# Performance work log

Measured on AMD Instinct MI355X. Metric: run time of the kernel, lower is better.

## Reference

```python
import jax, jax.numpy as jnp
import numpy as np

SEQ_LEN = 15
BATCH = 32
N_NODES = 5000
N_EDGES = 80000
IN_FEAT = 16
NHID = 2
G_FEAT = 1
HIDDEN = 512
N_LAYERS = 2


def setup_inputs() -> dict:
    key = jax.random.key(0)
    ks = jax.random.split(key, 16)
    x = jax.random.normal(ks[0], (SEQ_LEN, BATCH, N_NODES, IN_FEAT), dtype=jnp.float32)
    edge_index = jax.random.randint(ks[1], (2, N_EDGES), 0, N_NODES, dtype=jnp.int64)
    # per-timestep GCN weights (one GCN per timestep in the torch module)
    W1 = jax.random.normal(ks[2], (SEQ_LEN, IN_FEAT, NHID), dtype=jnp.float32) / np.sqrt(IN_FEAT)
    b1 = jnp.zeros((SEQ_LEN, NHID), dtype=jnp.float32)
    W2 = jax.random.normal(ks[3], (SEQ_LEN, NHID, G_FEAT), dtype=jnp.float32) / np.sqrt(NHID)
    b2 = jnp.zeros((SEQ_LEN, G_FEAT), dtype=jnp.float32)
    rnn_in = G_FEAT * N_NODES
    s_in = 1.0 / np.sqrt(HIDDEN)
    w_ih0 = jax.random.uniform(ks[4], (3 * HIDDEN, rnn_in), jnp.float32, -s_in, s_in)
    w_hh0 = jax.random.uniform(ks[5], (3 * HIDDEN, HIDDEN), jnp.float32, -s_in, s_in)
    b_ih0 = jax.random.uniform(ks[6], (3 * HIDDEN,), jnp.float32, -s_in, s_in)
    b_hh0 = jax.random.uniform(ks[7], (3 * HIDDEN,), jnp.float32, -s_in, s_in)
    w_ih1 = jax.random.uniform(ks[8], (3 * HIDDEN, HIDDEN), jnp.float32, -s_in, s_in)
    w_hh1 = jax.random.uniform(ks[9], (3 * HIDDEN, HIDDEN), jnp.float32, -s_in, s_in)
    b_ih1 = jax.random.uniform(ks[10], (3 * HIDDEN,), jnp.float32, -s_in, s_in)
    b_hh1 = jax.random.uniform(ks[11], (3 * HIDDEN,), jnp.float32, -s_in, s_in)
    return {"x": x, "edge_index": edge_index, "W1": W1, "b1": b1, "W2": W2, "b2": b2,
            "w_ih0": w_ih0, "w_hh0": w_hh0, "b_ih0": b_ih0, "b_hh0": b_hh0,
            "w_ih1": w_ih1, "w_hh1": w_hh1, "b_ih1": b_ih1, "b_hh1": b_hh1}


def _gcn_norm(edge_index, n_nodes):
    # PyG GCNConv: add self-loops, symmetric normalization
    loop = jnp.arange(n_nodes, dtype=edge_index.dtype)
    row = jnp.concatenate([edge_index[0], loop])  # source
    col = jnp.concatenate([edge_index[1], loop])  # target
    deg = jnp.zeros((n_nodes,), jnp.float32).at[col].add(1.0)
    dinv = deg ** -0.5  # deg >= 1 thanks to self-loops
    norm = dinv[row] * dinv[col]  # [E+N]
    return row, col, norm


def _propagate(h, row, col, norm, n_nodes):
    # h: [S,B,N,C] -> gather sources, scale, scatter-add to targets
    m = norm[:, None] * jnp.take(h, row, axis=2)  # [S,B,E,C]
    return jnp.zeros(h.shape[:2] + (n_nodes, h.shape[-1]), h.dtype).at[:, :, col, :].add(m)


def _gru_layer(inp, w_ih, w_hh, b_ih, b_hh):
    # inp: [S,B,I]; torch GRU cell math
    H = w_hh.shape[1]
    gi = jnp.einsum('sbi,gi->sbg', inp, w_ih) + b_ih  # [S,B,3H], precomputed input gates
    h0 = jnp.zeros((inp.shape[1], H), inp.dtype)

    def step(h, gi_t):
        gh = h @ w_hh.T + b_hh
        ir, iz, inn = jnp.split(gi_t, 3, axis=-1)
        hr, hz, hn = jnp.split(gh, 3, axis=-1)
        r = jax.nn.sigmoid(ir + hr)
        z = jax.nn.sigmoid(iz + hz)
        n = jnp.tanh(inn + r * hn)
        h_new = (1.0 - z) * n + z * h
        return h_new, h_new

    h_last, out = jax.lax.scan(step, h0, gi)
    return out, h_last


def reference(x, edge_index, W1, b1, W2, b2,
              w_ih0, w_hh0, b_ih0, b_hh0, w_ih1, w_hh1, b_ih1, b_hh1):
    S, B, N, F = x.shape
    row, col, norm = _gcn_norm(edge_index, N)
    # conv1: linear (per-timestep weights) -> propagate -> bias -> relu (dropout inactive in eval)
    h = jnp.einsum('sbnf,sfh->sbnh', x, W1)
    h = _propagate(h, row, col, norm, N) + b1[:, None, None, :]
    h = jax.nn.relu(h)
    # conv2
    h = jnp.einsum('sbnh,sho->sbno', h, W2)
    h = _propagate(h, row, col, norm, N) + b2[:, None, None, :]
    g = jnp.tanh(h).reshape(S, B, N * h.shape[-1])  # [S,B,rnn_in]
    out1, h1 = _gru_layer(g, w_ih0, w_hh0, b_ih0, b_hh0)
    out2, h2 = _gru_layer(out1, w_ih1, w_hh1, b_ih1, b_hh1)
    hn = jnp.stack([h1, h2])  # [n_layers,B,H]
    return out2, hn
```

## Files before the change

### kernel.cpp

```cpp
#include <hip/hip_runtime.h>

typedef unsigned int uint_t;

#define SEQ 15
#define BATCH 32
#define NNODES 5000
#define NEDGES 80000
#define INFEAT 16
#define HID 512
#define G3 1536
#define GRU_BLOCKS 256
#define BAR_INTS (32 * (2 * GRU_BLOCKS))

#define KSPLIT 9
#define KCHUNK 576
#define MROWS 480
#define LDSP 68

#define NSLC 16
#define PPAD 36

__device__ __forceinline__ float sigmoidf(float x){ return 1.0f / (1.0f + __expf(-x)); }

__global__ void k_init(int* counts, int* fill, int* bar,
                       float* h0a, float* h0b, float* h1a, float* h1b){
    int t = blockIdx.x * 256 + threadIdx.x;
    if (t < NNODES){ counts[t] = 0; fill[t] = 0; }
    if (t < BAR_INTS) bar[t] = 0;
    h0a[t] = 0.f; h0b[t] = 0.f; h1a[t] = 0.f; h1b[t] = 0.f;
}

__global__ void k_count(const int* ei, int* counts){
    int e = blockIdx.x * 256 + threadIdx.x;
    if (e < NEDGES) atomicAdd(&counts[ei[NEDGES + e]], 1);
}

__global__ void k_dinv(const int* counts, float* dinv){
    int n = blockIdx.x * 256 + threadIdx.x;
    if (n < NNODES) dinv[n] = rsqrtf(1.0f + (float)counts[n]);
}

__global__ void k_scan(const int* counts, int* offs){
    __shared__ int sdata[1024];
    int tid = threadIdx.x;
    int base = tid * 5;
    int loc[5]; int tot = 0;
    #pragma unroll
    for (int q = 0; q < 5; q++){
        int idx = base + q;
        int v = (idx < NNODES) ? counts[idx] : 0;
        loc[q] = tot; tot += v;
    }
    sdata[tid] = tot; __syncthreads();
    for (int off = 1; off < 1024; off <<= 1){
        int t = (tid >= off) ? sdata[tid - off] : 0;
        __syncthreads();
        sdata[tid] += t;
        __syncthreads();
    }
    int excl = sdata[tid] - tot;
    #pragma unroll
    for (int q = 0; q < 5; q++){
        int idx = base + q;
        if (idx < NNODES) offs[idx] = excl + loc[q];
    }
    if (tid == 1023) offs[NNODES] = sdata[1023];
}

__global__ void k_fill(const int* ei, const int* offs, int* fill, int* csr){
    int e = blockIdx.x * 256 + threadIdx.x;
    if (e < NEDGES){
        int c = ei[NEDGES + e];
        int p = offs[c] + atomicAdd(&fill[c], 1);
        csr[p] = ei[e];
    }
}

__global__ void k_conv1(const float* x, const float* W1, const float* dinv, float* h1s){
    int n = blockIdx.x * 256 + threadIdx.x;
    int b = blockIdx.y, s = blockIdx.z;
    if (n >= NNODES) return;
    float w[32];
    #pragma unroll
    for (int q = 0; q < 32; q++) w[q] = W1[s * 32 + q];
    size_t idx = ((size_t)(s * BATCH + b) * NNODES + n);
    const float4* xp = (const float4*)(x + idx * INFEAT);
    float4 u0 = xp[0], u1 = xp[1], u2 = xp[2], u3 = xp[3];
    float xs[16] = { u0.x,u0.y,u0.z,u0.w, u1.x,u1.y,u1.z,u1.w,
                     u2.x,u2.y,u2.z,u2.w, u3.x,u3.y,u3.z,u3.w };
    float a0 = 0.f, a1 = 0.f;
    #pragma unroll
    for (int f = 0; f < 16; f++){ a0 += xs[f] * w[2 * f]; a1 += xs[f] * w[2 * f + 1]; }
    float d = dinv[n];
    ((float2*)h1s)[idx] = make_float2(d * a0, d * a1);
}

__global__ void k_agg1(const float* h1s, const int* offs, const int* csr, const float* dinv,
                       const float* b1, const float* W2, float* h2s){
    int n = blockIdx.x * 256 + threadIdx.x;
    int b = blockIdx.y, s = blockIdx.z;
    if (n >= NNODES) return;
    size_t base = (size_t)(s * BATCH + b) * NNODES;
    const float2* hp = (const float2*)h1s + base;
    float2 self = hp[n];
    float a0 = self.x, a1 = self.y;
    int p1 = offs[n + 1];
    for (int p = offs[n]; p < p1; p++){
        float2 v = hp[csr[p]];
        a0 += v.x; a1 += v.y;
    }
    float d = dinv[n];
    float r0 = fmaxf(d * a0 + b1[s * 2 + 0], 0.f);
    float r1 = fmaxf(d * a1 + b1[s * 2 + 1], 0.f);
    float t2 = r0 * W2[s * 2 + 0] + r1 * W2[s * 2 + 1];
    h2s[base + n] = d * t2;
}

__global__ void k_agg2(const float* h2s, const int* offs, const int* csr, const float* dinv,
                       const float* b2, float* g){
    int n = blockIdx.x * 256 + threadIdx.x;
    int b = blockIdx.y, s = blockIdx.z;
    if (n >= NNODES) return;
    size_t base = (size_t)(s * BATCH + b) * NNODES;
    const float* hp = h2s + base;
    float a = hp[n];
    int p1 = offs[n + 1];
    for (int p = offs[n]; p < p1; p++) a += hp[csr[p]];
    g[base + n] = tanhf(dinv[n] * a + b2[s]);
}

__global__ __launch_bounds__(256) void k_gemm(const float* A, const float* W,
                                              float* part){
    __shared__ float As[16 * LDSP];
    __shared__ float Bs[16 * LDSP];
    int tid = threadIdx.x;
    int j0 = blockIdx.x * 64;
    int m0 = blockIdx.y * 64;
    int kz = blockIdx.z;
    int kbeg = kz * KCHUNK;
    int kend = kbeg + KCHUNK; if (kend > 5000) kend = 5000;
    int tm = tid >> 4, tn = tid & 15;
    int lr = tid >> 2;
    int lk = (tid & 3) * 4;
    float acc[4][4];
    #pragma unroll
    for (int i = 0; i < 4; i++)
        #pragma unroll
        for (int j = 0; j < 4; j++) acc[i][j] = 0.f;

    for (int k0 = kbeg; k0 < kend; k0 += 16){
        int m = m0 + lr;
        float4 av = make_float4(0.f, 0.f, 0.f, 0.f);
        if (m < MROWS && (k0 + lk) < 5000)
            av = *(const float4*)&A[(size_t)m * 5000 + k0 + lk];
        As[(lk + 0) * LDSP + lr] = av.x; As[(lk + 1) * LDSP + lr] = av.y;
        As[(lk + 2) * LDSP + lr] = av.z; As[(lk + 3) * LDSP + lr] = av.w;
        int j = j0 + lr;
        float4 bv = make_float4(0.f, 0.f, 0.f, 0.f);
        if ((k0 + lk) < 5000)
            bv = *(const float4*)&W[(size_t)j * 5000 + k0 + lk];
        Bs[(lk + 0) * LDSP + lr] = bv.x; Bs[(lk + 1) * LDSP + lr] = bv.y;
        Bs[(lk + 2) * LDSP + lr] = bv.z; Bs[(lk + 3) * LDSP + lr] = bv.w;
        __syncthreads();
        #pragma unroll
        for (int k = 0; k < 16; k++){
            float4 a = *(float4*)&As[k * LDSP + tm * 4];
            float4 bb = *(float4*)&Bs[k * LDSP + tn * 4];
            acc[0][0] += a.x * bb.x; acc[0][1] += a.x * bb.y; acc[0][2] += a.x * bb.z; acc[0][3] += a.x * bb.w;
            acc[1][0] += a.y * bb.x; acc[1][1] += a.y * bb.y; acc[1][2] += a.y * bb.z; acc[1][3] += a.y * bb.w;
            acc[2][0] += a.z * bb.x; acc[2][1] += a.z * bb.y; acc[2][2] += a.z * bb.z; acc[2][3] += a.z * bb.w;
            acc[3][0] += a.w * bb.x; acc[3][1] += a.w * bb.y; acc[3][2] += a.w * bb.z; acc[3][3] += a.w * bb.w;
        }
        __syncthreads();
    }
    size_t zbase = (size_t)kz * MROWS * G3;
    #pragma unroll
    for (int i = 0; i < 4; i++){
        int m = m0 + tm * 4 + i;
        if (m < MROWS){
            #pragma unroll
            for (int j = 0; j < 4; j++){
                int col = j0 + tn * 4 + j;
                part[zbase + (size_t)m * G3 + col] = acc[i][j];
            }
        }
    }
}

__global__ __launch_bounds__(256) void k_gred(const float* part, const float* bias, float* C){
    int idx = blockIdx.x * 256 + threadIdx.x;
    float s = bias[idx % G3];
    float sum = 0.f;
    #pragma unroll
    for (int z = 0; z < KSPLIT; z++)
        sum += part[(size_t)z * MROWS * G3 + idx];
    C[idx] = sum + s;
}

__device__ __forceinline__ void grid_barrier(int* bar, int phase){
    __syncthreads();
    if (threadIdx.x == 0){
        __threadfence();
        __hip_atomic_store(&bar[32 * blockIdx.x], phase,
                           __ATOMIC_RELAXED, __HIP_MEMORY_SCOPE_AGENT);
    }
    if (blockIdx.x == 0 && threadIdx.x < 64){
        int lane = threadIdx.x;
        for (;;){
            int mn = 0x7fffffff;
            #pragma unroll
            for (int q = 0; q < 4; q++){
                int v = __hip_atomic_load(&bar[32 * (lane + 64 * q)],
                                          __ATOMIC_RELAXED, __HIP_MEMORY_SCOPE_AGENT);
                mn = min(mn, v);
            }
            if (__all(mn >= phase)) break;
            __builtin_amdgcn_s_sleep(4);
        }
        __threadfence();
        #pragma unroll
        for (int q = 0; q < 4; q++)
            __hip_atomic_store(&bar[32 * (GRU_BLOCKS + lane + 64 * q)], phase,
                               __ATOMIC_RELAXED, __HIP_MEMORY_SCOPE_AGENT);
    }
    if (threadIdx.x == 0){
        while (__hip_atomic_load(&bar[32 * (GRU_BLOCKS + blockIdx.x)],
                                 __ATOMIC_RELAXED, __HIP_MEMORY_SCOPE_AGENT) < phase)
            __builtin_amdgcn_s_sleep(4);
        __threadfence();
    }
    __syncthreads();
}

template<int NR>
__device__ __forceinline__ void gemv_part(const float* __restrict__ h,
                                          const float* __restrict__ wsm0,
                                          float* __restrict__ part0, int bq, int ks){
    float acc[NR][4];
    #pragma unroll
    for (int r = 0; r < NR; r++){ acc[r][0] = acc[r][1] = acc[r][2] = acc[r][3] = 0.f; }
    #pragma unroll 2
    for (int j = 0; j < 8; j++){
        int k = ks * 4 + j * 64;
        float4 hv0 = *(const float4*)&h[(k + 0) * 32 + 4 * bq];
        float4 hv1 = *(const float4*)&h[(k + 1) * 32 + 4 * bq];
        float4 hv2 = *(const float4*)&h[(k + 2) * 32 + 4 * bq];
        float4 hv3 = *(const float4*)&h[(k + 3) * 32 + 4 * bq];
        #pragma unroll
        for (int r = 0; r < NR; r++){
            float4 w = *(const float4*)&wsm0[r * HID + k];
            acc[r][0] += w.x * hv0.x + w.y * hv1.x + w.z * hv2.x + w.w * hv3.x;
            acc[r][1] += w.x * hv0.y + w.y * hv1.y + w.z * hv2.y + w.w * hv3.y;
            acc[r][2] += w.x * hv0.z + w.y * hv1.z + w.z * hv2.z + w.w * hv3.z;
            acc[r][3] += w.x * hv0.w + w.y * hv1.w + w.z * hv2.w + w.w * hv3.w;
        }
    }
    #pragma unroll
    for (int r = 0; r < NR; r++)
        *(float4*)&part0[(r * NSLC + ks) * PPAD + 4 * bq] =
            make_float4(acc[r][0], acc[r][1], acc[r][2], acc[r][3]);
}

__global__ __launch_bounds__(512, 2) void k_gru(
        const float* __restrict__ gi0,
        const float* __restrict__ wih1, const float* __restrict__ whh0,
        const float* __restrict__ whh1,
        const float* __restrict__ bih1, const float* __restrict__ bhh0,
        const float* __restrict__ bhh1,
        float* __restrict__ h0a, float* __restrict__ h0b,
        float* __restrict__ h1a, float* __restrict__ h1b,
        float* __restrict__ out, int* bar){
    __shared__ float wsm[18 * HID];
    __shared__ float part[18 * NSLC * PPAD];
    __shared__ float ghl[18 * 32];
    __shared__ float outst[SEQ * 64];

    int tid = threadIdx.x;
    int i0 = blockIdx.x * 2;

    #pragma unroll
    for (int r = 0; r < 6; r++){
        int j = (r >> 1) * HID + i0 + (r & 1);
        for (int k = tid; k < HID; k += 512){
            wsm[r * HID + k]        = whh0[(size_t)j * HID + k];
            wsm[(6 + r) * HID + k]  = wih1[(size_t)j * HID + k];
            wsm[(12 + r) * HID + k] = whh1[(size_t)j * HID + k];
        }
    }
    __syncthreads();

    int t8  = tid & 255;
    int bq  = t8 & 7;
    int ks  = (t8 >> 3) & (NSLC - 1);
    int rh  = t8 >> 7;
    int l   = (tid >> 5) & 1, bb = tid & 31;
    int i   = i0 + l;
    float hs0 = 0.f, hs1 = 0.f;

    for (int p = 0; p <= SEQ; p++){
        const float* h0r = (p & 1) ? h0a : h0b;
        float*       h0w = (p & 1) ? h0b : h0a;
        const float* h1r = (p & 1) ? h1b : h1a;
        float*       h1w = (p & 1) ? h1a : h1b;

        float giR = 0.f, giZ = 0.f, giN = 0.f;
        if (tid < 64 && p < SEQ){
            const float* gi = gi0 + (size_t)(p * BATCH + bb) * G3;
            giR = gi[i]; giZ = gi[HID + i]; giN = gi[2 * HID + i];
        }

        if (tid < 256) gemv_part<6>(h0r, wsm + (rh * 6) * HID,
                                    part + (rh * 6) * NSLC * PPAD, bq, ks);
        else           gemv_part<3>(h1r, wsm + (12 + rh * 3) * HID,
                                    part + (12 + rh * 3) * NSLC * PPAD, bq, ks);
        __syncthreads();

        for (int o = tid; o < 18 * 32; o += 512){
            int row = o >> 5, b2 = o & 31;
            float sum = 0.f;
            #pragma unroll
            for (int q = 0; q < NSLC; q++) sum += part[(row * NSLC + q) * PPAD + b2];
            ghl[row * 32 + b2] = sum;
        }
        __syncthreads();

        if (tid < 64){
            if (p < SEQ){
                float ghr = ghl[(0 + l) * 32 + bb] + bhh0[i];
                float ghz = ghl[(2 + l) * 32 + bb] + bhh0[HID + i];
                float ghn = ghl[(4 + l) * 32 + bb] + bhh0[2 * HID + i];
                float rr = sigmoidf(giR + ghr);
                float zz = sigmoidf(giZ + ghz);
                float nn = tanhf(giN + rr * ghn);
                hs0 = (1.f - zz) * nn + zz * hs0;
                h0w[i * 32 + bb] = hs0;
            }
            if (p >= 1){
                float gir = ghl[(6 + l) * 32 + bb]  + bih1[i];
                float giz = ghl[(8 + l) * 32 + bb]  + bih1[HID + i];
                float gin = ghl[(10 + l) * 32 + bb] + bih1[2 * HID + i];
                float ghr = ghl[(12 + l) * 32 + bb] + bhh1[i];
                float ghz = ghl[(14 + l) * 32 + bb] + bhh1[HID + i];
                float ghn = ghl[(16 + l) * 32 + bb] + bhh1[2 * HID + i];
                float rr = sigmoidf(gir + ghr);
                float zz = sigmoidf(giz + ghz);
                float nn = tanhf(gin + rr * ghn);
                hs1 = (1.f - zz) * nn + zz * hs1;
                h1w[i * 32 + bb] = hs1;
                outst[(p - 1) * 64 + bb * 2 + l] = hs1;
            }
        }
        if (p < SEQ) grid_barrier(bar, p + 1);
    }

    __syncthreads();
    for (int o = tid; o < SEQ * 32; o += 512){
        int q = o >> 5, b2 = o & 31;
        float2 v = *(float2*)&outst[q * 64 + b2 * 2];
        *(float2*)&out[(size_t)(q * BATCH + b2) * HID + i0] = v;
    }
    if (tid < 64){
        out[SEQ * BATCH * HID + (size_t)bb * HID + i] = hs0;
        out[SEQ * BATCH * HID + BATCH * HID + (size_t)bb * HID + i] = hs1;
    }
}

extern "C" void kernel_launch(void* const* d_in, const int* in_sizes, int n_in,
                              void* d_out, int out_size, void* d_ws, size_t ws_size,
                              hipStream_t stream){
    (void)in_sizes; (void)n_in; (void)out_size; (void)ws_size;
    const float* x    = (const float*)d_in[0];
    const int*   ei   = (const int*)d_in[1];
    const float* W1   = (const float*)d_in[2];
    const float* b1   = (const float*)d_in[3];
    const float* W2   = (const float*)d_in[4];
    const float* b2   = (const float*)d_in[5];
    const float* wih0 = (const float*)d_in[6];
    const float* whh0 = (const float*)d_in[7];
    const float* bih0 = (const float*)d_in[8];
    const float* bhh0 = (const float*)d_in[9];
    const float* wih1 = (const float*)d_in[10];
    const float* whh1 = (const float*)d_in[11];
    const float* bih1 = (const float*)d_in[12];
    const float* bhh1 = (const float*)d_in[13];
    float* out = (float*)d_out;

    char* w = (char*)d_ws;
    auto alloc = [&](size_t bytes) -> char* {
        char* p = w; w += (bytes + 255) & ~(size_t)255; return p;
    };
    float* dinv   = (float*)alloc(NNODES * 4);
    int*   counts = (int*)  alloc(NNODES * 4);
    int*   offs   = (int*)  alloc((NNODES + 8) * 4);
    int*   fill   = (int*)  alloc(NNODES * 4);
    int*   csr    = (int*)  alloc(NEDGES * 4);
    int*   bar    = (int*)  alloc(BAR_INTS * 4);
    float* h0a    = (float*)alloc(HID * BATCH * 4);
    float* h0b    = (float*)alloc(HID * BATCH * 4);
    float* h1a    = (float*)alloc(HID * BATCH * 4);
    float* h1b    = (float*)alloc(HID * BATCH * 4);
    float* h1s    = (float*)alloc((size_t)SEQ * BATCH * NNODES * 2 * 4);
    float* h2s    = (float*)alloc((size_t)SEQ * BATCH * NNODES * 4);
    float* gbuf   = (float*)alloc((size_t)SEQ * BATCH * NNODES * 4);
    float* gi0    = (float*)alloc((size_t)SEQ * BATCH * G3 * 4);
    float* part   = h1s;

    k_init <<<64, 256, 0, stream>>>(counts, fill, bar, h0a, h0b, h1a, h1b);
    k_count<<<(NEDGES + 255) / 256, 256, 0, stream>>>(ei, counts);
    k_dinv <<<(NNODES + 255) / 256, 256, 0, stream>>>(counts, dinv);
    k_scan <<<1, 1024, 0, stream>>>(counts, offs);
    k_fill <<<(NEDGES + 255) / 256, 256, 0, stream>>>(ei, offs, fill, csr);

    dim3 gconv((NNODES + 255) / 256, BATCH, SEQ);
    k_conv1<<<gconv, 256, 0, stream>>>(x, W1, dinv, h1s);
    k_agg1 <<<gconv, 256, 0, stream>>>(h1s, offs, csr, dinv, b1, W2, h2s);
    k_agg2 <<<gconv, 256, 0, stream>>>(h2s, offs, csr, dinv, b2, gbuf);

    k_gemm<<<dim3(G3 / 64, 8, KSPLIT), 256, 0, stream>>>(gbuf, wih0, part);
    k_gred<<<(MROWS * G3) / 256, 256, 0, stream>>>(part, bih0, gi0);

    k_gru<<<GRU_BLOCKS, 512, 0, stream>>>(gi0, wih1, whh0, whh1, bih1, bhh0, bhh1,
                                          h0a, h0b, h1a, h1b, out, bar);
}
```

Measured before the change: 1.023 ms.

## Transpose GCN intermediates to node-major batch-contiguous layout for coalesced aggregation

Intermediate GCN buffers move from [S,B,N,C] to [S,N,B,C], so each wavefront aggregates one node across all 32 batches and each neighbour gather becomes a contiguous 256-byte (or 128-byte) row read. This replaces scattered per-thread random gathers and shares the CSR walk across the batch. k_agg2 splits the edges between half-wavefronts and transposes through LDS to write g in its original layout. In exchange, k_conv1's stores are strided and each wave processes nodes serially, so high-degree nodes can cause load imbalance.

```diff
diff --git a/kernel.cpp b/kernel.cpp
--- a/kernel.cpp
+++ b/kernel.cpp
@@ -20,6 +20,8 @@
 #define NSLC 16
 #define PPAD 36
 
+#define NT64 ((NNODES + 63) / 64)
+
 __device__ __forceinline__ float sigmoidf(float x){ return 1.0f / (1.0f + __expf(-x)); }
 
 __global__ void k_init(int* counts, int* fill, int* bar,
@@ -76,57 +78,94 @@
     }
 }
 
-__global__ void k_conv1(const float* x, const float* W1, const float* dinv, float* h1s){
-    int n = blockIdx.x * 256 + threadIdx.x;
-    int b = blockIdx.y, s = blockIdx.z;
+__global__ __launch_bounds__(256) void k_conv1(const float* __restrict__ x,
+        const float* __restrict__ W1, const float* __restrict__ dinv,
+        float* __restrict__ h1t){
+    int s = blockIdx.y;
+    int nn = threadIdx.x & 63;
+    int n  = blockIdx.x * 64 + nn;
+    int bq = threadIdx.x >> 6;
     if (n >= NNODES) return;
     float w[32];
     #pragma unroll
     for (int q = 0; q < 32; q++) w[q] = W1[s * 32 + q];
-    size_t idx = ((size_t)(s * BATCH + b) * NNODES + n);
-    const float4* xp = (const float4*)(x + idx * INFEAT);
-    float4 u0 = xp[0], u1 = xp[1], u2 = xp[2], u3 = xp[3];
-    float xs[16] = { u0.x,u0.y,u0.z,u0.w, u1.x,u1.y,u1.z,u1.w,
-                     u2.x,u2.y,u2.z,u2.w, u3.x,u3.y,u3.z,u3.w };
-    float a0 = 0.f, a1 = 0.f;
-    #pragma unroll
-    for (int f = 0; f < 16; f++){ a0 += xs[f] * w[2 * f]; a1 += xs[f] * w[2 * f + 1]; }
     float d = dinv[n];
-    ((float2*)h1s)[idx] = make_float2(d * a0, d * a1);
-}
-
-__global__ void k_agg1(const float* h1s, const int* offs, const int* csr, const float* dinv,
-                       const float* b1, const float* W2, float* h2s){
-    int n = blockIdx.x * 256 + threadIdx.x;
-    int b = blockIdx.y, s = blockIdx.z;
-    if (n >= NNODES) return;
-    size_t base = (size_t)(s * BATCH + b) * NNODES;
-    const float2* hp = (const float2*)h1s + base;
-    float2 self = hp[n];
-    float a0 = self.x, a1 = self.y;
-    int p1 = offs[n + 1];
-    for (int p = offs[n]; p < p1; p++){
-        float2 v = hp[csr[p]];
-        a0 += v.x; a1 += v.y;
-    }
-    float d = dinv[n];
-    float r0 = fmaxf(d * a0 + b1[s * 2 + 0], 0.f);
-    float r1 = fmaxf(d * a1 + b1[s * 2 + 1], 0.f);
-    float t2 = r0 * W2[s * 2 + 0] + r1 * W2[s * 2 + 1];
-    h2s[base + n] = d * t2;
-}
-
-__global__ void k_agg2(const float* h2s, const int* offs, const int* csr, const float* dinv,
-                       const float* b2, float* g){
-    int n = blockIdx.x * 256 + threadIdx.x;
-    int b = blockIdx.y, s = blockIdx.z;
-    if (n >= NNODES) return;
-    size_t base = (size_t)(s * BATCH + b) * NNODES;
-    const float* hp = h2s + base;
-    float a = hp[n];
-    int p1 = offs[n + 1];
-    for (int p = offs[n]; p < p1; p++) a += hp[csr[p]];
-    g[base + n] = tanhf(dinv[n] * a + b2[s]);
+    size_t sbase = (size_t)s * NNODES;
+    for (int j = 0; j < 8; j++){
+        int b = bq * 8 + j;
+        const float4* xp = (const float4*)(x + ((size_t)(s * BATCH + b) * NNODES + n) * INFEAT);
+        float4 u0 = xp[0], u1 = xp[1], u2 = xp[2], u3 = xp[3];
+        float xs[16] = { u0.x,u0.y,u0.z,u0.w, u1.x,u1.y,u1.z,u1.w,
+                         u2.x,u2.y,u2.z,u2.w, u3.x,u3.y,u3.z,u3.w };
+        float a0 = 0.f, a1 = 0.f;
+        #pragma unroll
+        for (int f = 0; f < 16; f++){ a0 += xs[f] * w[2 * f]; a1 += xs[f] * w[2 * f + 1]; }
+        ((float2*)h1t)[(sbase + n) * 32 + b] = make_float2(d * a0, d * a1);
+    }
+}
+
+__global__ __launch_bounds__(256) void k_agg1(const float* __restrict__ h1t,
+        const int* __restrict__ offs, const int* __restrict__ csr,
+        const float* __restrict__ dinv, const float* __restrict__ b1,
+        const float* __restrict__ W2, float* __restrict__ h2t){
+    int s = blockIdx.y;
+    int n0 = blockIdx.x * 64;
+    int wv = threadIdx.x >> 6, l = threadIdx.x & 63;
+    float w20 = W2[s * 2 + 0], w21 = W2[s * 2 + 1];
+    float bb1 = b1[s * 2 + (l & 1)];
+    size_t sbase = (size_t)s * NNODES;
+    for (int r = 0; r < 16; r++){
+        int n = n0 + wv + 4 * r;
+        if (n >= NNODES) continue;
+        const float* hp = h1t + (sbase + n) * 64;
+        float acc = hp[l];
+        int e0 = offs[n], e1 = offs[n + 1];
+        for (int p = e0; p < e1; p++){
+            int src = csr[p];
+            acc += h1t[(sbase + src) * 64 + l];
+        }
+        float d = dinv[n];
+        float val = fmaxf(d * acc + bb1, 0.f);
+        float oth = __shfl_xor(val, 1);
+        if ((l & 1) == 0)
+            h2t[(sbase + n) * 32 + (l >> 1)] = d * (val * w20 + oth * w21);
+    }
+}
+
+__global__ __launch_bounds__(256) void k_agg2(const float* __restrict__ h2t,
+        const int* __restrict__ offs, const int* __restrict__ csr,
+        const float* __restrict__ dinv, const float* __restrict__ b2,
+        float* __restrict__ g){
+    __shared__ float gst[64 * 33];
+    int s = blockIdx.y;
+    int n0 = blockIdx.x * 64;
+    int wv = threadIdx.x >> 6, l = threadIdx.x & 63;
+    int half = l >> 5, bl = l & 31;
+    float bs = b2[s];
+    size_t sbase = (size_t)s * NNODES;
+    for (int r = 0; r < 16; r++){
+        int n = n0 + wv + 4 * r;
+        if (n < NNODES){
+            float acc = half ? 0.f : h2t[(sbase + n) * 32 + bl];
+            int e0 = offs[n], e1 = offs[n + 1];
+            for (int p = e0 + half; p < e1; p += 2){
+                int src = csr[p];
+                acc += h2t[(sbase + src) * 32 + bl];
+            }
+            acc += __shfl_xor(acc, 32);
+            if (half == 0)
+                gst[(wv + 4 * r) * 33 + bl] = tanhf(dinv[n] * acc + bs);
+        }
+    }
+    __syncthreads();
+    #pragma unroll
+    for (int q = 0; q < 8; q++){
+        int flat = q * 256 + threadIdx.x;
+        int b = flat >> 6, nn = flat & 63;
+        int n = n0 + nn;
+        if (n < NNODES)
+            g[((size_t)s * BATCH + b) * NNODES + n] = gst[nn * 33 + b];
+    }
 }
 
 __global__ __launch_bounds__(256) void k_gemm(const float* A, const float* W,
@@ -399,11 +438,11 @@
     float* h0b    = (float*)alloc(HID * BATCH * 4);
     float* h1a    = (float*)alloc(HID * BATCH * 4);
     float* h1b    = (float*)alloc(HID * BATCH * 4);
-    float* h1s    = (float*)alloc((size_t)SEQ * BATCH * NNODES * 2 * 4);
-    float* h2s    = (float*)alloc((size_t)SEQ * BATCH * NNODES * 4);
+    float* h1t    = (float*)alloc((size_t)SEQ * NNODES * BATCH * 2 * 4);
+    float* h2t    = (float*)alloc((size_t)SEQ * NNODES * BATCH * 4);
     float* gbuf   = (float*)alloc((size_t)SEQ * BATCH * NNODES * 4);
     float* gi0    = (float*)alloc((size_t)SEQ * BATCH * G3 * 4);
-    float* part   = h1s;
+    float* part   = h1t;
 
     k_init <<<64, 256, 0, stream>>>(counts, fill, bar, h0a, h0b, h1a, h1b);
     k_count<<<(NEDGES + 255) / 256, 256, 0, stream>>>(ei, counts);
@@ -411,10 +450,10 @@
     k_scan <<<1, 1024, 0, stream>>>(counts, offs);
     k_fill <<<(NEDGES + 255) / 256, 256, 0, stream>>>(ei, offs, fill, csr);
 
-    dim3 gconv((NNODES + 255) / 256, BATCH, SEQ);
-    k_conv1<<<gconv, 256, 0, stream>>>(x, W1, dinv, h1s);
-    k_agg1 <<<gconv, 256, 0, stream>>>(h1s, offs, csr, dinv, b1, W2, h2s);
-    k_agg2 <<<gconv, 256, 0, stream>>>(h2s, offs, csr, dinv, b2, gbuf);
+    dim3 gtile(NT64, SEQ);
+    k_conv1<<<gtile, 256, 0, stream>>>(x, W1, dinv, h1t);
+    k_agg1 <<<gtile, 256, 0, stream>>>(h1t, offs, csr, dinv, b1, W2, h2t);
+    k_agg2 <<<gtile, 256, 0, stream>>>(h2t, offs, csr, dinv, b2, gbuf);
 
     k_gemm<<<dim3(G3 / 64, 8, KSPLIT), 256, 0, stream>>>(gbuf, wih0, part);
     k_gred<<<(MROWS * G3) / 256, 256, 0, stream>>>(part, bih0, gi0);
```

Result: faster. 887.6 us (-13.2%).
